# Performance work log

Measured on AMD Instinct MI355X. Metric: run time of the kernel, lower is better.

The kernel has to match this reference:

```python
import jax, jax.numpy as jnp
import numpy as np

NUM_EXPERTS = 8
TOP_K = 2
INIT_STD = 0.02


def setup_inputs() -> dict:
    key = jax.random.key(0)
    ks = jax.random.split(key, 10)
    B, S, H, I, SI, E = 2, 512, 2048, 1408, 5632, NUM_EXPERTS
    return {
        "hidden_states": jax.random.normal(ks[0], (B, S, H), jnp.float32),
        "gate_w": jax.random.normal(ks[1], (H, E), jnp.float32) * INIT_STD,
        "w_gate": jax.random.normal(ks[2], (E, H, I), jnp.float32) * INIT_STD,
        "w_up": jax.random.normal(ks[3], (E, H, I), jnp.float32) * INIT_STD,
        "w_down": jax.random.normal(ks[4], (E, I, H), jnp.float32) * INIT_STD,
        "sw_gate": jax.random.normal(ks[5], (H, SI), jnp.float32) * INIT_STD,
        "sw_up": jax.random.normal(ks[6], (H, SI), jnp.float32) * INIT_STD,
        "sw_down": jax.random.normal(ks[7], (SI, H), jnp.float32) * INIT_STD,
        "shared_gate_w": jax.random.normal(ks[8], (H, 1), jnp.float32) * INIT_STD,
    }


def reference(hidden_states, gate_w, w_gate, w_up, w_down, sw_gate, sw_up, sw_down, shared_gate_w):
    # Router: logits [B,S,E] in float32, softmax, top-k (norm_topk_prob=False)
    router_logits = (hidden_states @ gate_w).astype(jnp.float32)
    routing_weights = jax.nn.softmax(router_logits, axis=-1)
    top_w, sel = jax.lax.top_k(routing_weights, TOP_K)  # [B,S,K]
    # Scatter top-k weights back to dense per-expert weights [B,S,E]
    # (equals sum_k (sel==e) * top_w, as in the original masked accumulation)
    w = (jax.nn.one_hot(sel, NUM_EXPERTS, dtype=top_w.dtype) * top_w[..., None]).sum(axis=-2)
    # Dense loop over all experts, vectorized as batched einsum (same math)
    g = jnp.einsum('bsh,ehi->bsei', hidden_states, w_gate)
    u = jnp.einsum('bsh,ehi->bsei', hidden_states, w_up)
    expert_out = jnp.einsum('bsei,eih->bseh', jax.nn.silu(g) * u, w_down)  # [B,S,E,H]
    moe_out = jnp.einsum('bse,bseh->bsh', w.astype(hidden_states.dtype), expert_out)
    # Shared expert with sigmoid gate
    shared = (jax.nn.silu(hidden_states @ sw_gate) * (hidden_states @ sw_up)) @ sw_down
    shared = jax.nn.sigmoid(hidden_states @ shared_gate_w) * shared
    return moe_out + shared, router_logits
```

## Files before the change

### kernel.cpp

```cpp
#include <hip/hip_runtime.h>
#include <hip/hip_bf16.h>

#define T_TOK 1024
#define HDIM  2048
#define NEXP  8
#define IDIM  1408
#define SIDIM 5632
#define MAXSLOTS 24

typedef __attribute__((ext_vector_type(8))) short bf16x8;
typedef __attribute__((ext_vector_type(4))) float f32x4;
typedef unsigned short ushort_t;

__device__ __forceinline__ unsigned f2bf(float x) {
    unsigned u = __float_as_uint(x);
    return (u + 0x7fffu + ((u >> 16) & 1u)) >> 16;
}
__device__ __forceinline__ unsigned pack2(float a, float b) {
    return f2bf(a) | (f2bf(b) << 16);
}
__device__ __forceinline__ void async16(const void* g, void* l) {
    __builtin_amdgcn_global_load_lds(
        (const __attribute__((address_space(1))) void*)g,
        (__attribute__((address_space(3))) void*)l, 16, 0, 0);
}

__global__ __launch_bounds__(256) void conv_x(
    const float* __restrict__ src, ushort_t* __restrict__ dst)
{
    const int i = blockIdx.x * 256 + threadIdx.x;
    const float4* s = (const float4*)src + (size_t)i * 2;
    float4 a = s[0], b = s[1];
    union { ushort_t us[8]; uint4 v; } o;
    o.us[0] = (ushort_t)f2bf(a.x); o.us[1] = (ushort_t)f2bf(a.y);
    o.us[2] = (ushort_t)f2bf(a.z); o.us[3] = (ushort_t)f2bf(a.w);
    o.us[4] = (ushort_t)f2bf(b.x); o.us[5] = (ushort_t)f2bf(b.y);
    o.us[6] = (ushort_t)f2bf(b.z); o.us[7] = (ushort_t)f2bf(b.w);
    ((uint4*)dst)[i] = o.v;
}

__global__ __launch_bounds__(256) void conv_all(
    const float* __restrict__ wg, const float* __restrict__ wu,
    const float* __restrict__ wd, const float* __restrict__ swg,
    const float* __restrict__ swu, const float* __restrict__ swd,
    ushort_t* __restrict__ wtg, ushort_t* __restrict__ wtu,
    ushort_t* __restrict__ wtd, ushort_t* __restrict__ swtg,
    ushort_t* __restrict__ swtu, ushort_t* __restrict__ swtd)
{
    int id = blockIdx.x;
    const float* src; ushort_t* dst; int K, N, ktile, ntile;
    if (id < 11264) {
        const float* s0; ushort_t* d0;
        if (id < 5632) { s0 = wg; d0 = wtg; } else { s0 = wu; d0 = wtu; id -= 5632; }
        const int e = id / 704, t = id % 704;
        K = 2048; N = 1408;
        src = s0 + (size_t)e * K * N; dst = d0 + (size_t)e * K * N;
        ntile = t % 22; ktile = t / 22;
    } else if (id < 16896) {
        const int t2 = id - 11264;
        const int e = t2 / 704, t = t2 % 704;
        K = 1408; N = 2048;
        src = wd + (size_t)e * K * N; dst = wtd + (size_t)e * K * N;
        ntile = t % 32; ktile = t / 32;
    } else if (id < 22528) {
        int t2 = id - 16896; const float* s0; ushort_t* d0;
        if (t2 < 2816) { s0 = swg; d0 = swtg; } else { s0 = swu; d0 = swtu; t2 -= 2816; }
        K = 2048; N = 5632;
        src = s0; dst = d0;
        ntile = t2 % 88; ktile = t2 / 88;
    } else {
        const int t2 = id - 22528;
        K = 5632; N = 2048; src = swd; dst = swtd;
        ntile = t2 % 32; ktile = t2 / 32;
    }
    const int tid = threadIdx.x;
    __shared__ __align__(16) unsigned ldsw[32 * 68];
    const float* sp = src + (size_t)(ktile * 64) * N + ntile * 64;
    const int m = tid & 15;
    const int ph = tid >> 4;
#pragma unroll
    for (int h = 0; h < 2; ++h) {
        const int P = ph + h * 16;
        const float* r0 = sp + (size_t)(2 * P) * N + m * 4;
        f32x4 a = __builtin_nontemporal_load((const f32x4*)r0);
        f32x4 b = __builtin_nontemporal_load((const f32x4*)(r0 + N));
        uint4 u;
        u.x = pack2(a[0], b[0]); u.y = pack2(a[1], b[1]);
        u.z = pack2(a[2], b[2]); u.w = pack2(a[3], b[3]);
        *(uint4*)&ldsw[P * 68 + 4 * (m ^ (P >> 2))] = u;
    }
    __syncthreads();
    ushort_t* dp = dst + (size_t)(ntile * 64) * K + ktile * 64;
#pragma unroll
    for (int j = 0; j < 2; ++j) {
        const int c = tid + j * 256;
        const int row = c >> 3, kc = c & 7;
        const int base = 4 * ((row >> 2) ^ kc) + (row & 3);
        uint4 v;
        v.x = ldsw[(4 * kc + 0) * 68 + base];
        v.y = ldsw[(4 * kc + 1) * 68 + base];
        v.z = ldsw[(4 * kc + 2) * 68 + base];
        v.w = ldsw[(4 * kc + 3) * 68 + base];
        *(uint4*)(dp + (size_t)row * K + kc * 8) = v;
    }
}

__global__ __launch_bounds__(256) void router_kernel(
    const float* __restrict__ hs, const float* __restrict__ gw,
    const float* __restrict__ sgw, float* __restrict__ out_logits,
    float* __restrict__ w_dense, float* __restrict__ sgate,
    int* __restrict__ counts, int* __restrict__ tok_list)
{
    const int t = blockIdx.x;
    const int tid = threadIdx.x;
    const float* h = hs + (size_t)t * HDIM;
    float acc[9];
#pragma unroll
    for (int e = 0; e < 9; ++e) acc[e] = 0.f;
    for (int i = tid; i < HDIM; i += 256) {
        float hv = h[i];
        const float4* g4 = (const float4*)(gw + (size_t)i * NEXP);
        float4 g0 = g4[0], g1 = g4[1];
        acc[0] += hv * g0.x; acc[1] += hv * g0.y;
        acc[2] += hv * g0.z; acc[3] += hv * g0.w;
        acc[4] += hv * g1.x; acc[5] += hv * g1.y;
        acc[6] += hv * g1.z; acc[7] += hv * g1.w;
        acc[8] += hv * sgw[i];
    }
#pragma unroll
    for (int e = 0; e < 9; ++e)
        for (int off = 32; off > 0; off >>= 1)
            acc[e] += __shfl_down(acc[e], off, 64);
    __shared__ float lds[4][9];
    const int wid = tid >> 6, lane = tid & 63;
    if (lane == 0)
        for (int e = 0; e < 9; ++e) lds[wid][e] = acc[e];
    __syncthreads();
    if (tid == 0) {
        float l[9];
        for (int e = 0; e < 9; ++e)
            l[e] = lds[0][e] + lds[1][e] + lds[2][e] + lds[3][e];
        for (int e = 0; e < NEXP; ++e) out_logits[(size_t)t * NEXP + e] = l[e];
        float m = l[0];
        for (int e = 1; e < NEXP; ++e) m = fmaxf(m, l[e]);
        float p[NEXP], s = 0.f;
        for (int e = 0; e < NEXP; ++e) { p[e] = expf(l[e] - m); s += p[e]; }
        float inv = 1.f / s;
        for (int e = 0; e < NEXP; ++e) p[e] *= inv;
        int e0 = 0;
        for (int e = 1; e < NEXP; ++e) if (p[e] > p[e0]) e0 = e;
        int e1 = (e0 == 0) ? 1 : 0;
        for (int e = 0; e < NEXP; ++e) if (e != e0 && p[e] > p[e1]) e1 = e;
        for (int e = 0; e < NEXP; ++e)
            w_dense[(size_t)t * NEXP + e] = (e == e0) ? p[e0] : ((e == e1) ? p[e1] : 0.f);
        sgate[t] = 1.f / (1.f + expf(-l[8]));
        int p0 = atomicAdd(&counts[e0], 1); tok_list[e0 * T_TOK + p0] = t;
        int p1 = atomicAdd(&counts[e1], 1); tok_list[e1 * T_TOK + p1] = t;
    }
}

__global__ __launch_bounds__(64) void slot_kernel(
    const int* __restrict__ counts, int* __restrict__ slot_e,
    int* __restrict__ slot_rb, int* __restrict__ nslots)
{
    if (threadIdx.x == 0 && blockIdx.x == 0) {
        int ns = 0;
        for (int e = 0; e < NEXP; ++e)
            for (int b = 0; b < counts[e]; b += 128) {
                slot_e[ns] = e; slot_rb[ns] = b; ++ns;
            }
        nslots[0] = ns;
    }
}

__global__ __launch_bounds__(256) void gateup_all(
    const ushort_t* __restrict__ Xb,
    const ushort_t* __restrict__ swtg, const ushort_t* __restrict__ swtu,
    const ushort_t* __restrict__ wtg, const ushort_t* __restrict__ wtu,
    ushort_t* __restrict__ Ysh, ushort_t* __restrict__ Yr,
    const int* __restrict__ slot_e, const int* __restrict__ slot_rb,
    const int* __restrict__ counts, const int* __restrict__ nslots,
    const int* __restrict__ tok_list, const ushort_t* __restrict__ zerobuf)
{
    const int id = blockIdx.x;
    int n0, slot, e, rowbase, N, mode;
    if (id < 704) {
        mode = 1; n0 = (id % 88) * 64; slot = id / 88; e = 0; rowbase = 0; N = SIDIM;
    } else {
        mode = 0;
        const int id2 = id - 704;
        n0 = (id2 % 22) * 64; slot = id2 / 22;
        if (slot >= nslots[0]) return;
        e = slot_e[slot]; rowbase = slot_rb[slot]; N = IDIM;
    }
    const ushort_t* __restrict__ Wg = mode ? swtg : wtg + (size_t)e * HDIM * IDIM;
    const ushort_t* __restrict__ Wu = mode ? swtu : wtu + (size_t)e * HDIM * IDIM;
    ushort_t* __restrict__ Y = mode ? Ysh : Yr;
    const int K = HDIM;

    const int tid = threadIdx.x, lane = tid & 63, wid = tid >> 6;
    const int wr = (wid >> 1) * 64;
    const int wc = (wid & 1) * 32;
    const int fm = lane & 15, kg = lane >> 4;

    __shared__ int ltok[128];
    __shared__ __align__(16) ushort_t Xa[2][128 * 64];
    __shared__ __align__(16) ushort_t Bgs[2][64 * 64];
    __shared__ __align__(16) ushort_t Bus[2][64 * 64];

    if (tid < 128) {
        int tg;
        if (mode == 0) {
            int cnt = counts[e];
            tg = (rowbase + tid < cnt) ? tok_list[e * T_TOK + rowbase + tid] : -1;
        } else {
            tg = slot * 128 + tid;
        }
        ltok[tid] = tg;
    }
    __syncthreads();

    f32x4 ag[4][2], au[4][2];
#pragma unroll
    for (int a = 0; a < 4; ++a)
#pragma unroll
        for (int b = 0; b < 2; ++b) {
            ag[a][b] = f32x4{0.f, 0.f, 0.f, 0.f};
            au[a][b] = f32x4{0.f, 0.f, 0.f, 0.f};
        }

    const int koff = (((tid & 7) ^ ((tid >> 3) & 7))) * 8;
    const ushort_t* pA[4];
#pragma unroll
    for (int j = 0; j < 4; ++j) {
        const int r = (tid >> 3) + j * 32;
        const int tk = ltok[r];
        pA[j] = (tk >= 0) ? Xb + (size_t)tk * K + koff : zerobuf;
    }
    const ushort_t* pG[2];
    const ushort_t* pU[2];
#pragma unroll
    for (int j = 0; j < 2; ++j) {
        const int r = (tid >> 3) + j * 32;
        pG[j] = Wg + (size_t)(n0 + r) * K + koff;
        pU[j] = Wu + (size_t)(n0 + r) * K + koff;
    }

#define STAGE_GU(buf, k0)                                                   \
    {                                                                       \
        _Pragma("unroll")                                                   \
        for (int j = 0; j < 4; ++j)                                         \
            async16(pA[j] + (k0), &Xa[buf][(j * 256 + wid * 64) * 8]);      \
        _Pragma("unroll")                                                   \
        for (int j = 0; j < 2; ++j) {                                       \
            async16(pG[j] + (k0), &Bgs[buf][(j * 256 + wid * 64) * 8]);     \
            async16(pU[j] + (k0), &Bus[buf][(j * 256 + wid * 64) * 8]);     \
        }                                                                   \
    }

    const int NT = K / 64;
    STAGE_GU(0, 0);
    __syncthreads();

    for (int t = 0; t < NT; ++t) {
        const int cur = t & 1;
        if (t + 1 < NT) STAGE_GU(cur ^ 1, (t + 1) * 64);

#pragma unroll
        for (int ks = 0; ks < 2; ++ks) {
            const int kx = ((ks * 4 + kg) ^ (fm & 7)) * 8;
            bf16x8 af[4];
#pragma unroll
            for (int mt = 0; mt < 4; ++mt)
                af[mt] = *(const bf16x8*)&Xa[cur][(wr + mt * 16 + fm) * 64 + kx];
#pragma unroll
            for (int nt = 0; nt < 2; ++nt) {
                const int rb = (wc + nt * 16 + fm) * 64 + kx;
                bf16x8 bg = *(const bf16x8*)&Bgs[cur][rb];
                bf16x8 bu = *(const bf16x8*)&Bus[cur][rb];
#pragma unroll
                for (int mt = 0; mt < 4; ++mt) {
                    ag[mt][nt] = __builtin_amdgcn_mfma_f32_16x16x32_bf16(af[mt], bg, ag[mt][nt], 0, 0, 0);
                    au[mt][nt] = __builtin_amdgcn_mfma_f32_16x16x32_bf16(af[mt], bu, au[mt][nt], 0, 0, 0);
                }
            }
        }
        __syncthreads();
    }
#undef STAGE_GU

#pragma unroll
    for (int mt = 0; mt < 4; ++mt)
#pragma unroll
        for (int nt = 0; nt < 2; ++nt) {
            const int col = n0 + wc + nt * 16 + fm;
#pragma unroll
            for (int i = 0; i < 4; ++i) {
                const int row = wr + mt * 16 + kg * 4 + i;
                float g = ag[mt][nt][i], u = au[mt][nt][i];
                float yv = g / (1.f + expf(-g)) * u;
                Y[(size_t)(slot * 128 + row) * N + col] = (ushort_t)f2bf(yv);
            }
        }
}

__global__ __launch_bounds__(256) void down_all(
    const ushort_t* __restrict__ Ysh, const ushort_t* __restrict__ Yr,
    const ushort_t* __restrict__ swtd, const ushort_t* __restrict__ wtd,
    float* __restrict__ out,
    const int* __restrict__ slot_e, const int* __restrict__ slot_rb,
    const int* __restrict__ counts, const int* __restrict__ nslots,
    const int* __restrict__ tok_list, const float* __restrict__ w_dense,
    const float* __restrict__ sgate)
{
    const int id = blockIdx.x;
    int n0, slot, e, rowbase, K, kbase, ksteps, mode;
    const ushort_t* Yb;
    const ushort_t* Wd;
    if (id < 512) {
        mode = 1;
        n0 = (id & 15) * 128; slot = (id >> 4) & 7;
        const int z = id >> 7;
        K = SIDIM; kbase = z * 1408; ksteps = 22;
        e = 0; rowbase = 0;
        Yb = Ysh + (size_t)slot * 128 * K;
        Wd = swtd;
    } else {
        mode = 0;
        const int id2 = id - 512;
        n0 = (id2 & 15) * 128;
        const int rest = id2 >> 4;
        slot = rest >> 1;
        if (slot >= nslots[0]) return;
        const int z = rest & 1;
        K = IDIM; kbase = z * 704; ksteps = 11;
        e = slot_e[slot]; rowbase = slot_rb[slot];
        Yb = Yr + (size_t)slot * 128 * K;
        Wd = wtd + (size_t)e * IDIM * HDIM;
    }
    const int tid = threadIdx.x, lane = tid & 63, wid = tid >> 6;
    const int wr = (wid >> 1) * 64;
    const int wc = (wid & 1) * 64;
    const int fm = lane & 15, kg = lane >> 4;

    __shared__ int ltok[128];
    __shared__ float lw[128];
    __shared__ __align__(16) ushort_t Ya[2][128 * 64];
    __shared__ __align__(16) ushort_t Bd[2][128 * 64];

    if (tid < 128) {
        int tg; float wv;
        if (mode == 0) {
            int cnt = counts[e];
            if (rowbase + tid < cnt) {
                tg = tok_list[e * T_TOK + rowbase + tid];
                wv = w_dense[(size_t)tg * NEXP + e];
            } else { tg = -1; wv = 0.f; }
        } else {
            tg = slot * 128 + tid; wv = sgate[tg];
        }
        ltok[tid] = tg; lw[tid] = wv;
    }
    __syncthreads();

    f32x4 acc[4][4];
#pragma unroll
    for (int a = 0; a < 4; ++a)
#pragma unroll
        for (int b = 0; b < 4; ++b) acc[a][b] = f32x4{0.f, 0.f, 0.f, 0.f};

    const int koff = (((tid & 7) ^ ((tid >> 3) & 7))) * 8;
    const ushort_t* pY[4];
    const ushort_t* pW[4];
#pragma unroll
    for (int j = 0; j < 4; ++j) {
        const int r = (tid >> 3) + j * 32;
        pY[j] = Yb + (size_t)r * K + kbase + koff;
        pW[j] = Wd + (size_t)(n0 + r) * K + kbase + koff;
    }

#define STAGE_D(buf, k0)                                                    \
    {                                                                       \
        _Pragma("unroll")                                                   \
        for (int j = 0; j < 4; ++j) {                                       \
            async16(pY[j] + (k0), &Ya[buf][(j * 256 + wid * 64) * 8]);      \
            async16(pW[j] + (k0), &Bd[buf][(j * 256 + wid * 64) * 8]);      \
        }                                                                   \
    }

    STAGE_D(0, 0);
    __syncthreads();

    for (int s = 0; s < ksteps; ++s) {
        const int cur = s & 1;
        if (s + 1 < ksteps) STAGE_D(cur ^ 1, (s + 1) * 64);

#pragma unroll
        for (int ks = 0; ks < 2; ++ks) {
            const int kx = ((ks * 4 + kg) ^ (fm & 7)) * 8;
            bf16x8 af[4];
#pragma unroll
            for (int mt = 0; mt < 4; ++mt)
                af[mt] = *(const bf16x8*)&Ya[cur][(wr + mt * 16 + fm) * 64 + kx];
#pragma unroll
            for (int nt = 0; nt < 4; ++nt) {
                bf16x8 bf = *(const bf16x8*)&Bd[cur][(wc + nt * 16 + fm) * 64 + kx];
#pragma unroll
                for (int mt = 0; mt < 4; ++mt)
                    acc[mt][nt] = __builtin_amdgcn_mfma_f32_16x16x32_bf16(af[mt], bf, acc[mt][nt], 0, 0, 0);
            }
        }
        __syncthreads();
    }
#undef STAGE_D

#pragma unroll
    for (int mt = 0; mt < 4; ++mt)
#pragma unroll
        for (int nt = 0; nt < 4; ++nt) {
            const int col = n0 + wc + nt * 16 + fm;
#pragma unroll
            for (int i = 0; i < 4; ++i) {
                const int row = wr + mt * 16 + kg * 4 + i;
                const int tg = ltok[row];
                if (tg >= 0)
                    atomicAdd(out + (size_t)tg * HDIM + col, lw[row] * acc[mt][nt][i]);
            }
        }
}

extern "C" void kernel_launch(void* const* d_in, const int* in_sizes, int n_in,
                              void* d_out, int out_size, void* d_ws, size_t ws_size,
                              hipStream_t stream)
{
    const float* hs  = (const float*)d_in[0];
    const float* gw  = (const float*)d_in[1];
    const float* wg  = (const float*)d_in[2];
    const float* wu  = (const float*)d_in[3];
    const float* wd  = (const float*)d_in[4];
    const float* swg = (const float*)d_in[5];
    const float* swu = (const float*)d_in[6];
    const float* swd = (const float*)d_in[7];
    const float* sgw = (const float*)d_in[8];
    float* out = (float*)d_out;
    char* ws = (char*)d_ws;

    float* w_dense      = (float*)(ws + 0x00000);
    float* sgate        = (float*)(ws + 0x08000);
    int* counts         = (int*)(ws + 0x09000);
    int* nslots         = (int*)(ws + 0x09100);
    int* slot_e         = (int*)(ws + 0x09200);
    int* slot_rb        = (int*)(ws + 0x09300);
    int* tok_list       = (int*)(ws + 0x09400);
    ushort_t* zerobuf   = (ushort_t*)(ws + 0x11400);
    ushort_t* Xb        = (ushort_t*)(ws + 0x20000);
    ushort_t* Yr        = (ushort_t*)(ws + 0x420000);
    ushort_t* Ysh       = (ushort_t*)(ws + 0xC60000);
    ushort_t* wtg       = (ushort_t*)(ws + 0x1760000);
    ushort_t* wtu       = (ushort_t*)(ws + 0x4360000);
    ushort_t* wtd       = (ushort_t*)(ws + 0x6F60000);
    ushort_t* swtg      = (ushort_t*)(ws + 0x9B60000);
    ushort_t* swtu      = (ushort_t*)(ws + 0xB160000);
    ushort_t* swtd      = (ushort_t*)(ws + 0xC760000);
    float* out_logits = out + (size_t)T_TOK * HDIM;

    hipMemsetAsync(counts, 0, 256, stream);
    hipMemsetAsync(zerobuf, 0, 16384, stream);
    hipMemsetAsync(out, 0, (size_t)T_TOK * HDIM * sizeof(float), stream);

    conv_x<<<dim3(1024), dim3(256), 0, stream>>>(hs, Xb);
    conv_all<<<dim3(25344), dim3(256), 0, stream>>>(
        wg, wu, wd, swg, swu, swd, wtg, wtu, wtd, swtg, swtu, swtd);

    router_kernel<<<dim3(T_TOK), dim3(256), 0, stream>>>(
        hs, gw, sgw, out_logits, w_dense, sgate, counts, tok_list);
    slot_kernel<<<dim3(1), dim3(64), 0, stream>>>(counts, slot_e, slot_rb, nslots);

    gateup_all<<<dim3(704 + 22 * MAXSLOTS), dim3(256), 0, stream>>>(
        Xb, swtg, swtu, wtg, wtu, Ysh, Yr,
        slot_e, slot_rb, counts, nslots, tok_list, zerobuf);

    down_all<<<dim3(512 + 16 * MAXSLOTS * 2), dim3(256), 0, stream>>>(
        Ysh, Yr, swtd, wtd, out,
        slot_e, slot_rb, counts, nslots, tok_list, w_dense, sgate);
}
```

Measured before the change: 639.0 us.

## Keep two async stages in flight with vmcnt waits in GEMM loops

Rewrites the gate/up and down GEMM main loops to issue two LDS-direct global loads ahead and to wait with s_waitcnt vmcnt(8) plus raw s_barrier, instead of one stage ahead with __syncthreads. Sched barriers pin the compute and stage blocks in order. The aim is to hide global-load latency behind more MFMA work and to avoid the full waitcnt that __syncthreads implies. The hand-coded vmcnt count must match the number of loads issued per stage, and the peeled tail is more fragile when the K tile count is small or odd.

```diff
diff --git a/kernel.cpp b/kernel.cpp
--- a/kernel.cpp
+++ b/kernel.cpp
@@ -24,6 +24,11 @@
         (const __attribute__((address_space(1))) void*)g,
         (__attribute__((address_space(3))) void*)l, 16, 0, 0);
 }
+
+#define PIPE_BAR()    __builtin_amdgcn_s_barrier()
+#define SCHED_FENCE() __builtin_amdgcn_sched_barrier(0)
+#define WAIT_VM8()    asm volatile("s_waitcnt vmcnt(8)" ::: "memory")
+#define WAIT_VM0()    asm volatile("s_waitcnt vmcnt(0)" ::: "memory")
 
 __global__ __launch_bounds__(256) void conv_x(
     const float* __restrict__ src, ushort_t* __restrict__ dst)
@@ -246,48 +251,74 @@
         pU[j] = Wu + (size_t)(n0 + r) * K + koff;
     }
 
-#define STAGE_GU(buf, k0)                                                   \
+#define GU_STAGE(xp, gp, up, k0)                                            \
     {                                                                       \
         _Pragma("unroll")                                                   \
         for (int j = 0; j < 4; ++j)                                         \
-            async16(pA[j] + (k0), &Xa[buf][(j * 256 + wid * 64) * 8]);      \
+            async16(pA[j] + (k0), &(xp)[(j * 256 + wid * 64) * 8]);         \
         _Pragma("unroll")                                                   \
         for (int j = 0; j < 2; ++j) {                                       \
-            async16(pG[j] + (k0), &Bgs[buf][(j * 256 + wid * 64) * 8]);     \
-            async16(pU[j] + (k0), &Bus[buf][(j * 256 + wid * 64) * 8]);     \
+            async16(pG[j] + (k0), &(gp)[(j * 256 + wid * 64) * 8]);         \
+            async16(pU[j] + (k0), &(up)[(j * 256 + wid * 64) * 8]);         \
         }                                                                   \
     }
 
+#define GU_COMP(xa, bg, bu)                                                 \
+    {                                                                       \
+        _Pragma("unroll")                                                   \
+        for (int ks = 0; ks < 2; ++ks) {                                    \
+            const int kx = ((ks * 4 + kg) ^ (fm & 7)) * 8;                  \
+            bf16x8 af[4];                                                   \
+            _Pragma("unroll")                                               \
+            for (int mt = 0; mt < 4; ++mt)                                  \
+                af[mt] = *(const bf16x8*)&(xa)[(wr + mt * 16 + fm) * 64 + kx]; \
+            _Pragma("unroll")                                               \
+            for (int nt = 0; nt < 2; ++nt) {                                \
+                const int rb = (wc + nt * 16 + fm) * 64 + kx;               \
+                bf16x8 bgv = *(const bf16x8*)&(bg)[rb];                     \
+                bf16x8 buv = *(const bf16x8*)&(bu)[rb];                     \
+                _Pragma("unroll")                                           \
+                for (int mt = 0; mt < 4; ++mt) {                            \
+                    ag[mt][nt] = __builtin_amdgcn_mfma_f32_16x16x32_bf16(af[mt], bgv, ag[mt][nt], 0, 0, 0); \
+                    au[mt][nt] = __builtin_amdgcn_mfma_f32_16x16x32_bf16(af[mt], buv, au[mt][nt], 0, 0, 0); \
+                }                                                           \
+            }                                                               \
+        }                                                                   \
+    }
+
     const int NT = K / 64;
-    STAGE_GU(0, 0);
-    __syncthreads();
-
-    for (int t = 0; t < NT; ++t) {
-        const int cur = t & 1;
-        if (t + 1 < NT) STAGE_GU(cur ^ 1, (t + 1) * 64);
-
-#pragma unroll
-        for (int ks = 0; ks < 2; ++ks) {
-            const int kx = ((ks * 4 + kg) ^ (fm & 7)) * 8;
-            bf16x8 af[4];
-#pragma unroll
-            for (int mt = 0; mt < 4; ++mt)
-                af[mt] = *(const bf16x8*)&Xa[cur][(wr + mt * 16 + fm) * 64 + kx];
-#pragma unroll
-            for (int nt = 0; nt < 2; ++nt) {
-                const int rb = (wc + nt * 16 + fm) * 64 + kx;
-                bf16x8 bg = *(const bf16x8*)&Bgs[cur][rb];
-                bf16x8 bu = *(const bf16x8*)&Bus[cur][rb];
-#pragma unroll
-                for (int mt = 0; mt < 4; ++mt) {
-                    ag[mt][nt] = __builtin_amdgcn_mfma_f32_16x16x32_bf16(af[mt], bg, ag[mt][nt], 0, 0, 0);
-                    au[mt][nt] = __builtin_amdgcn_mfma_f32_16x16x32_bf16(af[mt], bu, au[mt][nt], 0, 0, 0);
-                }
-            }
-        }
-        __syncthreads();
-    }
-#undef STAGE_GU
+    GU_STAGE(Xa[0], Bgs[0], Bus[0], 0);
+    GU_STAGE(Xa[1], Bgs[1], Bus[1], 64);
+
+    int t = 0;
+    for (; t + 3 < NT; t += 2) {
+        WAIT_VM8(); PIPE_BAR(); SCHED_FENCE();
+        GU_COMP(Xa[0], Bgs[0], Bus[0]);
+        SCHED_FENCE(); PIPE_BAR(); SCHED_FENCE();
+        GU_STAGE(Xa[0], Bgs[0], Bus[0], (t + 2) * 64);
+
+        WAIT_VM8(); PIPE_BAR(); SCHED_FENCE();
+        GU_COMP(Xa[1], Bgs[1], Bus[1]);
+        SCHED_FENCE(); PIPE_BAR(); SCHED_FENCE();
+        GU_STAGE(Xa[1], Bgs[1], Bus[1], (t + 3) * 64);
+    }
+    if (t + 2 < NT) {
+        WAIT_VM8(); PIPE_BAR(); SCHED_FENCE();
+        GU_COMP(Xa[0], Bgs[0], Bus[0]);
+        SCHED_FENCE(); PIPE_BAR(); SCHED_FENCE();
+        GU_STAGE(Xa[0], Bgs[0], Bus[0], (t + 2) * 64);
+        WAIT_VM8(); PIPE_BAR(); SCHED_FENCE();
+        GU_COMP(Xa[1], Bgs[1], Bus[1]);
+        WAIT_VM0(); PIPE_BAR(); SCHED_FENCE();
+        GU_COMP(Xa[0], Bgs[0], Bus[0]);
+    } else {
+        WAIT_VM8(); PIPE_BAR(); SCHED_FENCE();
+        GU_COMP(Xa[0], Bgs[0], Bus[0]);
+        WAIT_VM0(); PIPE_BAR(); SCHED_FENCE();
+        GU_COMP(Xa[1], Bgs[1], Bus[1]);
+    }
+#undef GU_STAGE
+#undef GU_COMP
 
 #pragma unroll
     for (int mt = 0; mt < 4; ++mt)
@@ -379,40 +410,67 @@
         pW[j] = Wd + (size_t)(n0 + r) * K + kbase + koff;
     }
 
-#define STAGE_D(buf, k0)                                                    \
+#define D_STAGE(yp, bp, k0)                                                 \
     {                                                                       \
         _Pragma("unroll")                                                   \
         for (int j = 0; j < 4; ++j) {                                       \
-            async16(pY[j] + (k0), &Ya[buf][(j * 256 + wid * 64) * 8]);      \
-            async16(pW[j] + (k0), &Bd[buf][(j * 256 + wid * 64) * 8]);      \
+            async16(pY[j] + (k0), &(yp)[(j * 256 + wid * 64) * 8]);         \
+            async16(pW[j] + (k0), &(bp)[(j * 256 + wid * 64) * 8]);         \
         }                                                                   \
     }
 
-    STAGE_D(0, 0);
-    __syncthreads();
-
-    for (int s = 0; s < ksteps; ++s) {
-        const int cur = s & 1;
-        if (s + 1 < ksteps) STAGE_D(cur ^ 1, (s + 1) * 64);
-
-#pragma unroll
-        for (int ks = 0; ks < 2; ++ks) {
-            const int kx = ((ks * 4 + kg) ^ (fm & 7)) * 8;
-            bf16x8 af[4];
-#pragma unroll
-            for (int mt = 0; mt < 4; ++mt)
-                af[mt] = *(const bf16x8*)&Ya[cur][(wr + mt * 16 + fm) * 64 + kx];
-#pragma unroll
-            for (int nt = 0; nt < 4; ++nt) {
-                bf16x8 bf = *(const bf16x8*)&Bd[cur][(wc + nt * 16 + fm) * 64 + kx];
-#pragma unroll
-                for (int mt = 0; mt < 4; ++mt)
-                    acc[mt][nt] = __builtin_amdgcn_mfma_f32_16x16x32_bf16(af[mt], bf, acc[mt][nt], 0, 0, 0);
-            }
-        }
-        __syncthreads();
-    }
-#undef STAGE_D
+#define D_COMP(ya, bd)                                                      \
+    {                                                                       \
+        _Pragma("unroll")                                                   \
+        for (int ks = 0; ks < 2; ++ks) {                                    \
+            const int kx = ((ks * 4 + kg) ^ (fm & 7)) * 8;                  \
+            bf16x8 af[4];                                                   \
+            _Pragma("unroll")                                               \
+            for (int mt = 0; mt < 4; ++mt)                                  \
+                af[mt] = *(const bf16x8*)&(ya)[(wr + mt * 16 + fm) * 64 + kx]; \
+            _Pragma("unroll")                                               \
+            for (int nt = 0; nt < 4; ++nt) {                                \
+                bf16x8 bfv = *(const bf16x8*)&(bd)[(wc + nt * 16 + fm) * 64 + kx]; \
+                _Pragma("unroll")                                           \
+                for (int mt = 0; mt < 4; ++mt)                              \
+                    acc[mt][nt] = __builtin_amdgcn_mfma_f32_16x16x32_bf16(af[mt], bfv, acc[mt][nt], 0, 0, 0); \
+            }                                                               \
+        }                                                                   \
+    }
+
+    const int NT = ksteps;
+    D_STAGE(Ya[0], Bd[0], 0);
+    D_STAGE(Ya[1], Bd[1], 64);
+
+    int t = 0;
+    for (; t + 3 < NT; t += 2) {
+        WAIT_VM8(); PIPE_BAR(); SCHED_FENCE();
+        D_COMP(Ya[0], Bd[0]);
+        SCHED_FENCE(); PIPE_BAR(); SCHED_FENCE();
+        D_STAGE(Ya[0], Bd[0], (t + 2) * 64);
+
+        WAIT_VM8(); PIPE_BAR(); SCHED_FENCE();
+        D_COMP(Ya[1], Bd[1]);
+        SCHED_FENCE(); PIPE_BAR(); SCHED_FENCE();
+        D_STAGE(Ya[1], Bd[1], (t + 3) * 64);
+    }
+    if (t + 2 < NT) {
+        WAIT_VM8(); PIPE_BAR(); SCHED_FENCE();
+        D_COMP(Ya[0], Bd[0]);
+        SCHED_FENCE(); PIPE_BAR(); SCHED_FENCE();
+        D_STAGE(Ya[0], Bd[0], (t + 2) * 64);
+        WAIT_VM8(); PIPE_BAR(); SCHED_FENCE();
+        D_COMP(Ya[1], Bd[1]);
+        WAIT_VM0(); PIPE_BAR(); SCHED_FENCE();
+        D_COMP(Ya[0], Bd[0]);
+    } else {
+        WAIT_VM8(); PIPE_BAR(); SCHED_FENCE();
+        D_COMP(Ya[0], Bd[0]);
+        WAIT_VM0(); PIPE_BAR(); SCHED_FENCE();
+        D_COMP(Ya[1], Bd[1]);
+    }
+#undef D_STAGE
+#undef D_COMP
 
 #pragma unroll
     for (int mt = 0; mt < 4; ++mt)
```

Result: faster. 609.9 us (-4.6%).
